# Kernel optimization log

Hardware: AMD Instinct MI355X
Metric: run time of the kernel (lower is better)

Reference implementation:

```python
import jax, jax.numpy as jnp
import numpy as np

# Synthetic layered DAG: 8 node-layers of width N -> 7 masked dense layers.
B = 4096        # batch
N = 2048        # nodes per DAG layer (= in_features = out_features)
DEPTH = 7       # number of weight layers (len(L) - 1)
DENSITY = 0.25  # fraction of predecessor edges present (mask sparsity)


def setup_inputs() -> dict:
    key = jax.random.key(0)
    kx, kw, km = jax.random.split(key, 3)
    x = jax.random.normal(kx, (B, N), dtype=jnp.float32)
    # Mask M: [DEPTH, N+1, N]; random 0/1 edges, last row (bias) all ones.
    m = (jax.random.uniform(km, (DEPTH, N + 1, N)) < DENSITY).astype(jnp.float32)
    M = m.at[:, -1, :].set(1.0)
    # Kaiming-uniform per column: bound = 1/sqrt(nnz_j) (torch code's init),
    # nonzero only at masked positions (W initialized to zeros elsewhere).
    nnz = jnp.maximum(M.sum(axis=1, keepdims=True), 1.0)  # [DEPTH,1,N]
    u = jax.random.uniform(kw, (DEPTH, N + 1, N), minval=-1.0, maxval=1.0)
    W = (u / jnp.sqrt(nnz)) * M
    return {"x": x, "W": W, "M": M}


def reference(x, W, M):
    # activations buffer semantics collapse to a per-layer chain because each
    # layer's preds are exactly the previous DAG layer; sinks = last layer.
    def step(acts, wm):
        w, m = wm  # [N+1, N] each
        h = jnp.concatenate(
            [acts, jnp.ones((acts.shape[0], 1), acts.dtype)], axis=1)  # [B, N+1]
        acts = jax.nn.relu(h @ (m * w))  # masked dense matmul + ReLU
        return acts, None

    out, _ = jax.lax.scan(step, x, (W, M))
    return out  # [B, N] activations of sink nodes
```

## Files before the change

### kernel.cpp

```cpp
#include <hip/hip_runtime.h>
#include <hip/hip_bf16.h>

typedef __bf16 bf16_t;
typedef __bf16 v8bf __attribute__((ext_vector_type(8)));
typedef __bf16 v4bf __attribute__((ext_vector_type(4)));
typedef float  v4f  __attribute__((ext_vector_type(4)));

#define B_ROWS 4096
#define N_COLS 2048
#define K_FULL 2049
#define KK     2048
#define DEPTH  7

#define BM 128
#define BN 128
#define BK 64
#define NKT (KK / BK)

__global__ __launch_bounds__(256) void wt_kernel(const float* __restrict__ W,
                                                 bf16_t* __restrict__ Wt,
                                                 float* __restrict__ Bias) {
  __shared__ float t[64][129];
  const int l  = blockIdx.z;
  const int k0 = blockIdx.x * 128;
  const int n0 = blockIdx.y * 64;
  const int tid = threadIdx.x;
  const int r   = tid >> 4;
  const int c4  = (tid & 15) * 4;
  const float* Wl = W + (size_t)l * K_FULL * N_COLS;
#pragma unroll
  for (int it = 0; it < 8; ++it) {
    const int kk = r + it * 16;
    const float4 v = *(const float4*)&Wl[(size_t)(k0 + kk) * N_COLS + n0 + c4];
    t[c4 + 0][kk] = v.x;
    t[c4 + 1][kk] = v.y;
    t[c4 + 2][kk] = v.z;
    t[c4 + 3][kk] = v.w;
  }
  if (k0 == 0 && tid < 16) {
    *(float4*)&Bias[(size_t)l * N_COLS + n0 + tid * 4] =
        *(const float4*)&Wl[(size_t)KK * N_COLS + n0 + tid * 4];
  }
  __syncthreads();
  bf16_t* Wtl = Wt + (size_t)l * N_COLS * KK;
  const int g = tid & 15;
#pragma unroll
  for (int it = 0; it < 4; ++it) {
    const int n = r + it * 16;
    v8bf o;
#pragma unroll
    for (int j = 0; j < 8; ++j) o[j] = (bf16_t)t[n][g * 8 + j];
    *(v8bf*)&Wtl[(size_t)(n0 + n) * KK + k0 + g * 8] = o;
  }
}

__global__ __launch_bounds__(256) void init_kernel(const float* __restrict__ x,
                                                   bf16_t* __restrict__ A0) {
  const int c4 = (blockIdx.x * 256 + threadIdx.x) * 4;
  const int r  = blockIdx.y;
  const float4 v = *(const float4*)&x[(size_t)r * N_COLS + c4];
  v4bf o;
  o[0] = (bf16_t)v.x; o[1] = (bf16_t)v.y; o[2] = (bf16_t)v.z; o[3] = (bf16_t)v.w;
  *(v4bf*)&A0[(size_t)r * N_COLS + c4] = o;
}

__global__ __launch_bounds__(512, 4) void gemm_kernel(
    const bf16_t* __restrict__ A, const bf16_t* __restrict__ Bt,
    const float* __restrict__ bias,
    bf16_t* __restrict__ Cn, float* __restrict__ Co) {
  __shared__ __align__(16) char smem[65536];

  const int bid = blockIdx.x;
  const int swz = (bid & 7) * 64 + (bid >> 3);
  const int bx  = swz & 15;
  const int by  = swz >> 4;

  const int tid  = threadIdx.x;
  const int wave = tid >> 6;
  const int lane = tid & 63;
  const int q    = wave & 3;
  const int kgrp = wave >> 2;
  const int m0 = by * BM;
  const int n0 = bx * BN;
  const int wm = (q & 1) * 64;
  const int wn = (q >> 1) * 64;
  const int quad = lane >> 4;
  const int l16  = lane & 15;

  int aoff[2], boff[2];
#pragma unroll
  for (int c = 0; c < 2; ++c) {
    const int gg  = c * 512 + tid;
    const int row = gg >> 3;
    const int sc  = ((gg & 7) ^ (row & 7)) << 3;
    aoff[c] = (m0 + row) * KK + sc;
    boff[c] = (n0 + row) * KK + sc;
  }

  const int X = ((kgrp * 4 + quad) ^ (l16 & 7)) << 4;
  int ra[4], rb[4];
#pragma unroll
  for (int i = 0; i < 4; ++i) ra[i] = (wm + i * 16 + l16) * 128 + X;
#pragma unroll
  for (int j = 0; j < 4; ++j) rb[j] = (wn + j * 16 + l16) * 128 + X;

  auto stage = [&](int b, int kb) {
    char* dA = smem + b * 32768;
    char* dB = dA + 16384;
#pragma unroll
    for (int c = 0; c < 2; ++c) {
      __builtin_amdgcn_global_load_lds(
          (const __attribute__((address_space(1))) void*)(A + aoff[c] + kb),
          (__attribute__((address_space(3))) void*)(dA + c * 8192 + tid * 16),
          16, 0, 0);
    }
#pragma unroll
    for (int c = 0; c < 2; ++c) {
      __builtin_amdgcn_global_load_lds(
          (const __attribute__((address_space(1))) void*)(Bt + boff[c] + kb),
          (__attribute__((address_space(3))) void*)(dB + c * 8192 + tid * 16),
          16, 0, 0);
    }
  };

  v4f acc[4][4] = {};

  stage(0, 0);
  __syncthreads();

#pragma unroll 2
  for (int kt = 0; kt < NKT; ++kt) {
    const int cur = kt & 1;
    if (kt + 1 < NKT) stage(cur ^ 1, (kt + 1) * BK);

    const char* ab = smem + cur * 32768;
    const char* bb = ab + 16384;
    v8bf af[4], bfr[4];
#pragma unroll
    for (int i = 0; i < 4; ++i) af[i]  = *(const v8bf*)(ab + ra[i]);
#pragma unroll
    for (int j = 0; j < 4; ++j) bfr[j] = *(const v8bf*)(bb + rb[j]);
#pragma unroll
    for (int i = 0; i < 4; ++i)
#pragma unroll
      for (int j = 0; j < 4; ++j)
        acc[i][j] = __builtin_amdgcn_mfma_f32_16x16x32_bf16(af[i], bfr[j],
                                                            acc[i][j], 0, 0, 0);
    __syncthreads();
  }

  float* red = (float*)smem;
#pragma unroll
  for (int j = 0; j < 4; ++j) {
    if (kgrp == 0) {
      *(v4f*)(red + q * 4096 + 2 * 1024 + j * 256 + lane * 4) = acc[2][j];
      *(v4f*)(red + q * 4096 + 3 * 1024 + j * 256 + lane * 4) = acc[3][j];
    } else {
      *(v4f*)(red + q * 4096 + 0 * 1024 + j * 256 + lane * 4) = acc[0][j];
      *(v4f*)(red + q * 4096 + 1 * 1024 + j * 256 + lane * 4) = acc[1][j];
    }
  }
  __syncthreads();
#pragma unroll
  for (int j = 0; j < 4; ++j) {
    if (kgrp == 0) {
      acc[0][j] += *(const v4f*)(red + q * 4096 + 0 * 1024 + j * 256 + lane * 4);
      acc[1][j] += *(const v4f*)(red + q * 4096 + 1 * 1024 + j * 256 + lane * 4);
    } else {
      acc[2][j] += *(const v4f*)(red + q * 4096 + 2 * 1024 + j * 256 + lane * 4);
      acc[3][j] += *(const v4f*)(red + q * 4096 + 3 * 1024 + j * 256 + lane * 4);
    }
  }

  float bv[4];
#pragma unroll
  for (int j = 0; j < 4; ++j) bv[j] = bias[n0 + wn + j * 16 + l16];
  const int i0 = kgrp * 2;
#pragma unroll
  for (int ii = 0; ii < 2; ++ii) {
#pragma unroll
    for (int j = 0; j < 4; ++j) {
      v4f a = (kgrp == 0) ? acc[ii][j] : acc[2 + ii][j];
#pragma unroll
      for (int r = 0; r < 4; ++r) {
        float v = a[r] + bv[j];
        v = v > 0.0f ? v : 0.0f;
        const int row = m0 + wm + (i0 + ii) * 16 + quad * 4 + r;
        const int col = n0 + wn + j * 16 + l16;
        if (Co) Co[(size_t)row * N_COLS + col] = v;
        else    Cn[(size_t)row * N_COLS + col] = (bf16_t)v;
      }
    }
  }
}

extern "C" void kernel_launch(void* const* d_in, const int* in_sizes, int n_in,
                              void* d_out, int out_size, void* d_ws, size_t ws_size,
                              hipStream_t stream) {
  const float* x = (const float*)d_in[0];
  const float* W = (const float*)d_in[1];
  float* out = (float*)d_out;

  char* ws = (char*)d_ws;
  const size_t wtBytes = (size_t)DEPTH * N_COLS * KK * sizeof(bf16_t);
  const size_t aBytes  = (size_t)B_ROWS * N_COLS * sizeof(bf16_t);
  bf16_t* Wt   = (bf16_t*)ws;
  bf16_t* A0   = (bf16_t*)(ws + wtBytes);
  bf16_t* A1   = (bf16_t*)(ws + wtBytes + aBytes);
  float*  Bias = (float*)(ws + wtBytes + 2 * aBytes);

  wt_kernel<<<dim3(KK / 128, N_COLS / 64, DEPTH), 256, 0, stream>>>(W, Wt, Bias);
  init_kernel<<<dim3(N_COLS / 4 / 256, B_ROWS), 256, 0, stream>>>(x, A0);

  bf16_t* bufs[2] = {A0, A1};
  for (int l = 0; l < DEPTH; ++l) {
    const bf16_t* Ain = bufs[l & 1];
    bf16_t* Aout      = bufs[(l + 1) & 1];
    const bf16_t* Bl  = Wt + (size_t)l * N_COLS * KK;
    const float* bl   = Bias + (size_t)l * N_COLS;
    const bool last   = (l == DEPTH - 1);
    gemm_kernel<<<dim3((B_ROWS / BM) * (N_COLS / BN)), 512, 0, stream>>>(
        Ain, Bl, bl, last ? nullptr : Aout, last ? out : nullptr);
  }
}
```

Baseline: 469.8 us.

## Use 16 waves with 32x32 output tiles instead of split-K wave groups

Changes the GEMM block from 8 waves (4 output quadrants × 2 K-groups with an LDS reduction) to 16 waves, each owning a 32x32 output sub-tile over the full BK slice. This removes the cross-wave LDS reduction and its extra barrier. Each thread now issues one A and one B async load per stage. The trade-off is smaller per-wave tiles, so each LDS fragment feeds fewer MFMAs, and 1024-thread blocks carry heavier barrier and register pressure constraints.

```diff
diff --git a/kernel.cpp b/kernel.cpp
--- a/kernel.cpp
+++ b/kernel.cpp
@@ -64,7 +64,7 @@
   *(v4bf*)&A0[(size_t)r * N_COLS + c4] = o;
 }
 
-__global__ __launch_bounds__(512, 4) void gemm_kernel(
+__global__ __launch_bounds__(1024, 8) void gemm_kernel(
     const bf16_t* __restrict__ A, const bf16_t* __restrict__ Bt,
     const float* __restrict__ bias,
     bf16_t* __restrict__ Cn, float* __restrict__ Co) {
@@ -78,52 +78,37 @@
   const int tid  = threadIdx.x;
   const int wave = tid >> 6;
   const int lane = tid & 63;
-  const int q    = wave & 3;
-  const int kgrp = wave >> 2;
   const int m0 = by * BM;
   const int n0 = bx * BN;
-  const int wm = (q & 1) * 64;
-  const int wn = (q >> 1) * 64;
+  const int wm = (wave >> 2) * 32;
+  const int wn = (wave & 3) * 32;
   const int quad = lane >> 4;
   const int l16  = lane & 15;
 
-  int aoff[2], boff[2];
+  const int srow = tid >> 3;
+  const int sc   = ((tid & 7) ^ (srow & 7)) << 3;
+  const int aoff = (m0 + srow) * KK + sc;
+  const int boff = (n0 + srow) * KK + sc;
+
+  int ra[2], rb[2], X[2];
 #pragma unroll
-  for (int c = 0; c < 2; ++c) {
-    const int gg  = c * 512 + tid;
-    const int row = gg >> 3;
-    const int sc  = ((gg & 7) ^ (row & 7)) << 3;
-    aoff[c] = (m0 + row) * KK + sc;
-    boff[c] = (n0 + row) * KK + sc;
-  }
-
-  const int X = ((kgrp * 4 + quad) ^ (l16 & 7)) << 4;
-  int ra[4], rb[4];
+  for (int i = 0; i < 2; ++i) ra[i] = (wm + i * 16 + l16) * 128;
 #pragma unroll
-  for (int i = 0; i < 4; ++i) ra[i] = (wm + i * 16 + l16) * 128 + X;
+  for (int j = 0; j < 2; ++j) rb[j] = (wn + j * 16 + l16) * 128;
 #pragma unroll
-  for (int j = 0; j < 4; ++j) rb[j] = (wn + j * 16 + l16) * 128 + X;
+  for (int ks = 0; ks < 2; ++ks) X[ks] = ((ks * 4 + quad) ^ (l16 & 7)) << 4;
 
   auto stage = [&](int b, int kb) {
     char* dA = smem + b * 32768;
-    char* dB = dA + 16384;
-#pragma unroll
-    for (int c = 0; c < 2; ++c) {
-      __builtin_amdgcn_global_load_lds(
-          (const __attribute__((address_space(1))) void*)(A + aoff[c] + kb),
-          (__attribute__((address_space(3))) void*)(dA + c * 8192 + tid * 16),
-          16, 0, 0);
-    }
-#pragma unroll
-    for (int c = 0; c < 2; ++c) {
-      __builtin_amdgcn_global_load_lds(
-          (const __attribute__((address_space(1))) void*)(Bt + boff[c] + kb),
-          (__attribute__((address_space(3))) void*)(dB + c * 8192 + tid * 16),
-          16, 0, 0);
-    }
+    __builtin_amdgcn_global_load_lds(
+        (const __attribute__((address_space(1))) void*)(A + aoff + kb),
+        (__attribute__((address_space(3))) void*)(dA + tid * 16), 16, 0, 0);
+    __builtin_amdgcn_global_load_lds(
+        (const __attribute__((address_space(1))) void*)(Bt + boff + kb),
+        (__attribute__((address_space(3))) void*)(dA + 16384 + tid * 16), 16, 0, 0);
   };
 
-  v4f acc[4][4] = {};
+  v4f acc[2][2] = {};
 
   stage(0, 0);
   __syncthreads();
@@ -135,57 +120,35 @@
 
     const char* ab = smem + cur * 32768;
     const char* bb = ab + 16384;
-    v8bf af[4], bfr[4];
 #pragma unroll
-    for (int i = 0; i < 4; ++i) af[i]  = *(const v8bf*)(ab + ra[i]);
+    for (int ks = 0; ks < 2; ++ks) {
+      v8bf af[2], bfr[2];
 #pragma unroll
-    for (int j = 0; j < 4; ++j) bfr[j] = *(const v8bf*)(bb + rb[j]);
+      for (int i = 0; i < 2; ++i) af[i]  = *(const v8bf*)(ab + ra[i] + X[ks]);
 #pragma unroll
-    for (int i = 0; i < 4; ++i)
+      for (int j = 0; j < 2; ++j) bfr[j] = *(const v8bf*)(bb + rb[j] + X[ks]);
 #pragma unroll
-      for (int j = 0; j < 4; ++j)
-        acc[i][j] = __builtin_amdgcn_mfma_f32_16x16x32_bf16(af[i], bfr[j],
-                                                            acc[i][j], 0, 0, 0);
+      for (int i = 0; i < 2; ++i)
+#pragma unroll
+        for (int j = 0; j < 2; ++j)
+          acc[i][j] = __builtin_amdgcn_mfma_f32_16x16x32_bf16(af[i], bfr[j],
+                                                              acc[i][j], 0, 0, 0);
+    }
     __syncthreads();
   }
 
-  float* red = (float*)smem;
+  float bv[2];
 #pragma unroll
-  for (int j = 0; j < 4; ++j) {
-    if (kgrp == 0) {
-      *(v4f*)(red + q * 4096 + 2 * 1024 + j * 256 + lane * 4) = acc[2][j];
-      *(v4f*)(red + q * 4096 + 3 * 1024 + j * 256 + lane * 4) = acc[3][j];
-    } else {
-      *(v4f*)(red + q * 4096 + 0 * 1024 + j * 256 + lane * 4) = acc[0][j];
-      *(v4f*)(red + q * 4096 + 1 * 1024 + j * 256 + lane * 4) = acc[1][j];
-    }
-  }
-  __syncthreads();
+  for (int j = 0; j < 2; ++j) bv[j] = bias[n0 + wn + j * 16 + l16];
 #pragma unroll
-  for (int j = 0; j < 4; ++j) {
-    if (kgrp == 0) {
-      acc[0][j] += *(const v4f*)(red + q * 4096 + 0 * 1024 + j * 256 + lane * 4);
-      acc[1][j] += *(const v4f*)(red + q * 4096 + 1 * 1024 + j * 256 + lane * 4);
-    } else {
-      acc[2][j] += *(const v4f*)(red + q * 4096 + 2 * 1024 + j * 256 + lane * 4);
-      acc[3][j] += *(const v4f*)(red + q * 4096 + 3 * 1024 + j * 256 + lane * 4);
-    }
-  }
-
-  float bv[4];
+  for (int i = 0; i < 2; ++i) {
 #pragma unroll
-  for (int j = 0; j < 4; ++j) bv[j] = bias[n0 + wn + j * 16 + l16];
-  const int i0 = kgrp * 2;
-#pragma unroll
-  for (int ii = 0; ii < 2; ++ii) {
-#pragma unroll
-    for (int j = 0; j < 4; ++j) {
-      v4f a = (kgrp == 0) ? acc[ii][j] : acc[2 + ii][j];
+    for (int j = 0; j < 2; ++j) {
 #pragma unroll
       for (int r = 0; r < 4; ++r) {
-        float v = a[r] + bv[j];
+        float v = acc[i][j][r] + bv[j];
         v = v > 0.0f ? v : 0.0f;
-        const int row = m0 + wm + (i0 + ii) * 16 + quad * 4 + r;
+        const int row = m0 + wm + i * 16 + quad * 4 + r;
         const int col = n0 + wn + j * 16 + l16;
         if (Co) Co[(size_t)row * N_COLS + col] = v;
         else    Cn[(size_t)row * N_COLS + col] = (bf16_t)v;
@@ -219,7 +182,7 @@
     const bf16_t* Bl  = Wt + (size_t)l * N_COLS * KK;
     const float* bl   = Bias + (size_t)l * N_COLS;
     const bool last   = (l == DEPTH - 1);
-    gemm_kernel<<<dim3((B_ROWS / BM) * (N_COLS / BN)), 512, 0, stream>>>(
+    gemm_kernel<<<dim3((B_ROWS / BM) * (N_COLS / BN)), 1024, 0, stream>>>(
         Ain, Bl, bl, last ? nullptr : Aout, last ? out : nullptr);
   }
 }
```

Result: no change. 473.3 us (+0.7%).

## Drop intra-block split-K, use 4 waves with BK=32 tiles

Applied to the files above, without the earlier changes.

Before, the GEMM split each 64-wide K slice between two groups of four waves and summed the halves in LDS at the end. Now each block has four waves, each owning a 64x64 output tile, and the K tile shrinks to 32 with an XOR swizzle over four 16-byte chunks to match. LDS use is halved and the final LDS reduction and its barrier are removed. In exchange there are twice as many K iterations, each ending in a barrier, and fewer waves per block to hide load latency.

```diff
diff --git a/kernel.cpp b/kernel.cpp
--- a/kernel.cpp
+++ b/kernel.cpp
@@ -14,7 +14,7 @@
 
 #define BM 128
 #define BN 128
-#define BK 64
+#define BK 32
 #define NKT (KK / BK)
 
 __global__ __launch_bounds__(256) void wt_kernel(const float* __restrict__ W,
@@ -64,11 +64,11 @@
   *(v4bf*)&A0[(size_t)r * N_COLS + c4] = o;
 }
 
-__global__ __launch_bounds__(512, 4) void gemm_kernel(
+__global__ __launch_bounds__(256, 4) void gemm_kernel(
     const bf16_t* __restrict__ A, const bf16_t* __restrict__ Bt,
     const float* __restrict__ bias,
     bf16_t* __restrict__ Cn, float* __restrict__ Co) {
-  __shared__ __align__(16) char smem[65536];
+  __shared__ __align__(16) char smem[32768];
 
   const int bid = blockIdx.x;
   const int swz = (bid & 7) * 64 + (bid >> 3);
@@ -78,47 +78,44 @@
   const int tid  = threadIdx.x;
   const int wave = tid >> 6;
   const int lane = tid & 63;
-  const int q    = wave & 3;
-  const int kgrp = wave >> 2;
   const int m0 = by * BM;
   const int n0 = bx * BN;
-  const int wm = (q & 1) * 64;
-  const int wn = (q >> 1) * 64;
+  const int wm = (wave >> 1) * 64;
+  const int wn = (wave & 1) * 64;
   const int quad = lane >> 4;
   const int l16  = lane & 15;
 
   int aoff[2], boff[2];
 #pragma unroll
   for (int c = 0; c < 2; ++c) {
-    const int gg  = c * 512 + tid;
-    const int row = gg >> 3;
-    const int sc  = ((gg & 7) ^ (row & 7)) << 3;
+    const int gg  = c * 256 + tid;
+    const int row = gg >> 2;
+    const int sc  = ((gg & 3) ^ (row & 3)) << 3;
     aoff[c] = (m0 + row) * KK + sc;
     boff[c] = (n0 + row) * KK + sc;
   }
 
-  const int X = ((kgrp * 4 + quad) ^ (l16 & 7)) << 4;
+  const int X = ((quad ^ (l16 & 3)) << 4);
   int ra[4], rb[4];
 #pragma unroll
-  for (int i = 0; i < 4; ++i) ra[i] = (wm + i * 16 + l16) * 128 + X;
+  for (int i = 0; i < 4; ++i) ra[i] = (wm + i * 16 + l16) * 64 + X;
 #pragma unroll
-  for (int j = 0; j < 4; ++j) rb[j] = (wn + j * 16 + l16) * 128 + X;
+  for (int j = 0; j < 4; ++j) rb[j] = (wn + j * 16 + l16) * 64 + X;
 
   auto stage = [&](int b, int kb) {
-    char* dA = smem + b * 32768;
-    char* dB = dA + 16384;
+    char* dA = smem + b * 16384;
 #pragma unroll
     for (int c = 0; c < 2; ++c) {
       __builtin_amdgcn_global_load_lds(
           (const __attribute__((address_space(1))) void*)(A + aoff[c] + kb),
-          (__attribute__((address_space(3))) void*)(dA + c * 8192 + tid * 16),
+          (__attribute__((address_space(3))) void*)(dA + c * 4096 + tid * 16),
           16, 0, 0);
     }
 #pragma unroll
     for (int c = 0; c < 2; ++c) {
       __builtin_amdgcn_global_load_lds(
           (const __attribute__((address_space(1))) void*)(Bt + boff[c] + kb),
-          (__attribute__((address_space(3))) void*)(dB + c * 8192 + tid * 16),
+          (__attribute__((address_space(3))) void*)(dA + 8192 + c * 4096 + tid * 16),
           16, 0, 0);
     }
   };
@@ -133,8 +130,8 @@
     const int cur = kt & 1;
     if (kt + 1 < NKT) stage(cur ^ 1, (kt + 1) * BK);
 
-    const char* ab = smem + cur * 32768;
-    const char* bb = ab + 16384;
+    const char* ab = smem + cur * 16384;
+    const char* bb = ab + 8192;
     v8bf af[4], bfr[4];
 #pragma unroll
     for (int i = 0; i < 4; ++i) af[i]  = *(const v8bf*)(ab + ra[i]);
@@ -149,43 +146,18 @@
     __syncthreads();
   }
 
-  float* red = (float*)smem;
-#pragma unroll
-  for (int j = 0; j < 4; ++j) {
-    if (kgrp == 0) {
-      *(v4f*)(red + q * 4096 + 2 * 1024 + j * 256 + lane * 4) = acc[2][j];
-      *(v4f*)(red + q * 4096 + 3 * 1024 + j * 256 + lane * 4) = acc[3][j];
-    } else {
-      *(v4f*)(red + q * 4096 + 0 * 1024 + j * 256 + lane * 4) = acc[0][j];
-      *(v4f*)(red + q * 4096 + 1 * 1024 + j * 256 + lane * 4) = acc[1][j];
-    }
-  }
-  __syncthreads();
-#pragma unroll
-  for (int j = 0; j < 4; ++j) {
-    if (kgrp == 0) {
-      acc[0][j] += *(const v4f*)(red + q * 4096 + 0 * 1024 + j * 256 + lane * 4);
-      acc[1][j] += *(const v4f*)(red + q * 4096 + 1 * 1024 + j * 256 + lane * 4);
-    } else {
-      acc[2][j] += *(const v4f*)(red + q * 4096 + 2 * 1024 + j * 256 + lane * 4);
-      acc[3][j] += *(const v4f*)(red + q * 4096 + 3 * 1024 + j * 256 + lane * 4);
-    }
-  }
-
   float bv[4];
 #pragma unroll
   for (int j = 0; j < 4; ++j) bv[j] = bias[n0 + wn + j * 16 + l16];
-  const int i0 = kgrp * 2;
 #pragma unroll
-  for (int ii = 0; ii < 2; ++ii) {
+  for (int i = 0; i < 4; ++i) {
 #pragma unroll
     for (int j = 0; j < 4; ++j) {
-      v4f a = (kgrp == 0) ? acc[ii][j] : acc[2 + ii][j];
 #pragma unroll
       for (int r = 0; r < 4; ++r) {
-        float v = a[r] + bv[j];
+        float v = acc[i][j][r] + bv[j];
         v = v > 0.0f ? v : 0.0f;
-        const int row = m0 + wm + (i0 + ii) * 16 + quad * 4 + r;
+        const int row = m0 + wm + i * 16 + quad * 4 + r;
         const int col = n0 + wn + j * 16 + l16;
         if (Co) Co[(size_t)row * N_COLS + col] = v;
         else    Cn[(size_t)row * N_COLS + col] = (bf16_t)v;
@@ -219,7 +191,7 @@
     const bf16_t* Bl  = Wt + (size_t)l * N_COLS * KK;
     const float* bl   = Bias + (size_t)l * N_COLS;
     const bool last   = (l == DEPTH - 1);
-    gemm_kernel<<<dim3((B_ROWS / BM) * (N_COLS / BN)), 512, 0, stream>>>(
+    gemm_kernel<<<dim3((B_ROWS / BM) * (N_COLS / BN)), 256, 0, stream>>>(
         Ain, Bl, bl, last ? nullptr : Aout, last ? out : nullptr);
   }
 }
```

Measured after the change: 517.7 us. +10.2%, slower.
